# Performance work log

Hardware: AMD Instinct MI355X
Metric: run time of the kernel (lower is better)

## Reference

```python
import jax, jax.numpy as jnp
import numpy as np

K_NEIGH = 16  # ball-query neighborhood size


def pdist2(a, b):
    # (B,N,3),(B,M,3) -> (B,N,M) squared euclidean distances
    aa = jnp.sum(a * a, -1)[:, :, None]
    bb = jnp.sum(b * b, -1)[:, None, :]
    return jnp.maximum(aa + bb - 2.0 * jnp.einsum('bnd,bmd->bnm', a, b), 0.0)


def fps(xyz, npoint):
    # furthest point sampling, xyz (B,N,3) -> idx (B,npoint) int32
    B, N, _ = xyz.shape

    def body(carry, _):
        dist, far = carry
        centroid = xyz[jnp.arange(B), far]  # (B,3)
        d = jnp.sum((xyz - centroid[:, None, :]) ** 2, -1)
        dist = jnp.minimum(dist, d)
        nxt = jnp.argmax(dist, axis=1).astype(jnp.int32)
        return (dist, nxt), far

    init = (jnp.full((B, N), 1e10, xyz.dtype), jnp.zeros((B,), jnp.int32))
    _, idxs = jax.lax.scan(body, init, None, length=npoint)
    return idxs.T  # (B, npoint)


def gather(x, idx):
    # x (B,N,C), idx (B,S) -> (B,S,C)
    return jnp.take_along_axis(x, idx[:, :, None], axis=1)


def lae_conv(xyz, fea, W, b, A, radius):
    # LAE-Conv: ball-query (K nearest capped to radius, out-of-ball -> self),
    # pointwise feature transform, attention over neighbors from coord offsets.
    B, N, _ = xyz.shape
    d2 = pdist2(xyz, xyz)
    negd, idx = jax.lax.top_k(-d2, K_NEIGH)          # (B,N,K)
    in_ball = (-negd) <= radius * radius
    self_idx = jnp.broadcast_to(jnp.arange(N, dtype=idx.dtype)[None, :, None], idx.shape)
    idx = jnp.where(in_ball, idx, self_idx)
    g_xyz = jnp.take_along_axis(xyz[:, None], idx[..., None], axis=2) - xyz[:, :, None, :]  # (B,N,K,3)
    g_fea = jnp.take_along_axis(fea[:, None], idx[..., None], axis=2)                        # (B,N,K,Cin)
    h = jnp.einsum('bnkc,co->bnko', g_fea, W) + b    # (B,N,K,Cout)
    alpha = jax.nn.softmax(jnp.einsum('bnkd,d->bnk', g_xyz, A), axis=-1)
    return jax.nn.relu(jnp.einsum('bnk,bnko->bno', alpha, h))


def self_attn(fea, Wq, Wk, Wv):
    # non-local self-attention block with additive merge (PSAB)
    q, k, v = fea @ Wq, fea @ Wk, fea @ Wv
    a = jax.nn.softmax(jnp.einsum('bnc,bmc->bnm', q, k), axis=-1)
    return jnp.einsum('bnm,bmc->bnc', a, v) + fea


def fp_interp(xyz_d, xyz_s, fea_d, fea_s):
    # pointnet feature propagation: 3-NN inverse-distance interp + skip concat
    d2 = pdist2(xyz_d, xyz_s)
    negd, idx = jax.lax.top_k(-d2, 3)
    w = 1.0 / jnp.maximum(-negd, 1e-10)
    w = w / jnp.sum(w, -1, keepdims=True)
    g = jnp.take_along_axis(fea_s[:, None], idx[..., None], axis=2)  # (B,Nd,3,C)
    interp = jnp.einsum('bnk,bnkc->bnc', w, g)
    return jnp.concatenate([fea_d, interp], axis=-1)


def pan_forward(xyz, W0, b0, A0, W1, b1, A1, W2, b2, A2, W3, b3, A3, W4, b4, A4,
                W5, b5, A5, W6, b6, A6, Wq1, Wk1, Wv1, Wq2, Wk2, Wv2, Wq3, Wk3, Wv3, Wf, bf):
    fea0 = lae_conv(xyz, xyz, W0, b0, A0, 0.06)       # (B,N,64)
    idx1 = fps(xyz, 512)
    xyz1, fea1 = gather(xyz, idx1), gather(fea0, idx1)
    fea1 = lae_conv(xyz1, fea1, W1, b1, A1, 0.12)     # (B,512,128)
    idx2 = fps(xyz1, 128)
    xyz2, fea2 = gather(xyz1, idx2), gather(fea1, idx2)
    fea2 = lae_conv(xyz2, fea2, W2, b2, A2, 0.3)      # (B,128,256)
    fea2 = self_attn(fea2, Wq1, Wk1, Wv1)
    idx3 = fps(xyz2, 64)
    xyz3, fea3 = gather(xyz2, idx3), gather(fea2, idx3)
    fea3 = lae_conv(xyz3, fea3, W3, b3, A3, 0.5)      # (B,64,512)
    fea3 = self_attn(fea3, Wq2, Wk2, Wv2)
    fea2 = fp_interp(xyz2, xyz3, fea2, fea3)          # (B,128,768)
    fea2 = lae_conv(xyz2, fea2, W4, b4, A4, 0.3)      # (B,128,256)
    fea2 = self_attn(fea2, Wq3, Wk3, Wv3)
    fea1 = fp_interp(xyz1, xyz2, fea1, fea2)          # (B,512,384)
    fea1 = lae_conv(xyz1, fea1, W5, b5, A5, 0.12)     # (B,512,256)
    fea0 = fp_interp(xyz, xyz1, fea0, fea1)           # (B,N,320)
    fea0 = lae_conv(xyz, fea0, W6, b6, A6, 0.06)      # (B,N,128)
    out = fea0 @ Wf + bf                              # (B,N,num_class)
    return out.transpose(0, 2, 1)                     # (B,num_class,N)


def setup_inputs() -> dict:
    key = jax.random.key(0)
    B, N, NUM_CLASS = 4, 4096, 13
    ks = iter(jax.random.split(key, 64))

    def lin(cin, cout):
        return jax.random.normal(next(ks), (cin, cout), jnp.float32) / np.sqrt(cin).astype(np.float32)

    inp = {'xyz': jax.random.uniform(next(ks), (B, N, 3), jnp.float32)}
    lae_dims = [(3, 64), (64, 128), (128, 256), (256, 512), (768, 256), (384, 256), (320, 128)]
    for i, (ci, co) in enumerate(lae_dims):
        inp[f'W{i}'] = lin(ci, co)
        inp[f'b{i}'] = jnp.zeros((co,), jnp.float32)
        inp[f'A{i}'] = jax.random.normal(next(ks), (3,), jnp.float32)
    for j, c in zip((1, 2, 3), (256, 512, 256)):
        inp[f'Wq{j}'] = lin(c, c)
        inp[f'Wk{j}'] = lin(c, c)
        inp[f'Wv{j}'] = lin(c, c)
    inp['Wf'] = lin(128, NUM_CLASS)
    inp['bf'] = jnp.zeros((NUM_CLASS,), jnp.float32)
    return inp


def reference(xyz, W0, b0, A0, W1, b1, A1, W2, b2, A2, W3, b3, A3, W4, b4, A4,
              W5, b5, A5, W6, b6, A6, Wq1, Wk1, Wv1, Wq2, Wk2, Wv2, Wq3, Wk3, Wv3, Wf, bf):
    return pan_forward(xyz, W0, b0, A0, W1, b1, A1, W2, b2, A2, W3, b3, A3, W4, b4, A4,
                       W5, b5, A5, W6, b6, A6, Wq1, Wk1, Wv1, Wq2, Wk2, Wv2, Wq3, Wk3, Wv3, Wf, bf)
```

## Files before the change

### kernel.cpp

```cpp
#include <hip/hip_runtime.h>
#include <math.h>

#define NB 4

typedef unsigned long long u64;

#define CSWAP(a, b)                                          \
  {                                                          \
    u64 _mn = (b < a) ? b : a;                               \
    u64 _mx = (b < a) ? a : b;                               \
    a = _mn;                                                 \
    b = _mx;                                                 \
  }

__device__ __forceinline__ void knn16_search(const float* __restrict__ xb, int N, int n,
                                             int lane, u64* lists, u64* win) {
#pragma clang fp contract(off)
  float qx = xb[n * 3 + 0], qy = xb[n * 3 + 1], qz = xb[n * 3 + 2];
  float qq = qx * qx + qy * qy + qz * qz;
  const u64 SENT = ((u64)0x7F800000u << 32) | (unsigned)lane;
  u64 k0 = SENT, k1 = SENT, k2 = SENT, k3 = SENT, k4 = SENT, k5 = SENT, k6 = SENT,
      k7 = SENT, k8 = SENT, k9 = SENT, k10 = SENT, k11 = SENT, k12 = SENT, k13 = SENT,
      k14 = SENT, k15 = SENT;
  int rounds = N >> 6;
  for (int j = 0; j < rounds; ++j) {
    int m = j * 64 + lane;
    float cx = xb[m * 3 + 0], cy = xb[m * 3 + 1], cz = xb[m * 3 + 2];
    float cc = cx * cx + cy * cy + cz * cz;
    float ab = qx * cx + qy * cy + qz * cz;
    float d2 = fmaxf(qq + cc - 2.0f * ab, 0.0f);
    u64 key = ((u64)__float_as_uint(d2) << 32) | (unsigned)m;
    if (key < k15) {
      k15 = key;
      CSWAP(k14, k15); CSWAP(k13, k14); CSWAP(k12, k13); CSWAP(k11, k12);
      CSWAP(k10, k11); CSWAP(k9, k10);  CSWAP(k8, k9);   CSWAP(k7, k8);
      CSWAP(k6, k7);   CSWAP(k5, k6);   CSWAP(k4, k5);   CSWAP(k3, k4);
      CSWAP(k2, k3);   CSWAP(k1, k2);   CSWAP(k0, k1);
    }
  }
  lists[0 * 64 + lane] = k0;   lists[1 * 64 + lane] = k1;
  lists[2 * 64 + lane] = k2;   lists[3 * 64 + lane] = k3;
  lists[4 * 64 + lane] = k4;   lists[5 * 64 + lane] = k5;
  lists[6 * 64 + lane] = k6;   lists[7 * 64 + lane] = k7;
  lists[8 * 64 + lane] = k8;   lists[9 * 64 + lane] = k9;
  lists[10 * 64 + lane] = k10; lists[11 * 64 + lane] = k11;
  lists[12 * 64 + lane] = k12; lists[13 * 64 + lane] = k13;
  lists[14 * 64 + lane] = k14; lists[15 * 64 + lane] = k15;
  __syncthreads();
  int head = 0;
  u64 outk = 0;
  for (int r = 0; r < 16; ++r) {
    u64 h = lists[head * 64 + lane];
    u64 mn = h;
#pragma unroll
    for (int mask = 32; mask; mask >>= 1) {
      u64 o = __shfl_xor(mn, mask);
      if (o < mn) mn = o;
    }
    if (h == mn) head++;
    if (lane == r) outk = mn;
  }
  if (lane < 16) win[lane] = outk;
  __syncthreads();
}

__device__ __forceinline__ void lae_alphas(const float* __restrict__ xb, int n,
                                           const int* idv, const float* __restrict__ A,
                                           float* al) {
  float ax = A[0], ay = A[1], az = A[2];
  float qx = xb[n * 3 + 0], qy = xb[n * 3 + 1], qz = xb[n * 3 + 2];
  float mx = -3.0e38f;
#pragma unroll
  for (int k = 0; k < 16; ++k) {
    float gx = xb[idv[k] * 3 + 0] - qx;
    float gy = xb[idv[k] * 3 + 1] - qy;
    float gz = xb[idv[k] * 3 + 2] - qz;
    float s = gx * ax + gy * ay + gz * az;
    al[k] = s;
    mx = fmaxf(mx, s);
  }
  float sum = 0.0f;
#pragma unroll
  for (int k = 0; k < 16; ++k) { al[k] = expf(al[k] - mx); sum += al[k]; }
#pragma unroll
  for (int k = 0; k < 16; ++k) al[k] = al[k] / sum;
}

template <int NT, int PTS, int NPT>
__device__ __forceinline__ void fps_body(const float* __restrict__ xyz, int N, int npoint,
                                         int* __restrict__ idx_out,
                                         float* __restrict__ xyz_out, u64* smem, int b,
                                         int tid) {
#pragma clang fp contract(off)
  constexpr int NW = NT / 64;
  constexpr int NG = NT / 16;
  u64* rk = smem;
  int* hist = (int*)(smem + 2 * NG);
  float* sxyz = (float*)(hist + 512);
  const float* xb = xyz + (size_t)b * N * 3;
  for (int i = tid; i < 3 * N; i += NT) sxyz[i] = xb[i];
  float px[PTS], py[PTS], pz[PTS], dist[PTS];
#pragma unroll
  for (int p = 0; p < PTS; ++p) {
    int pt = tid + p * NT;
    px[p] = xb[pt * 3 + 0];
    py[p] = xb[pt * 3 + 1];
    pz[p] = xb[pt * 3 + 2];
    dist[p] = 1e10f;
  }
  __syncthreads();
  int far = 0;
  float cx = sxyz[0], cy = sxyz[1], cz = sxyz[2];
  for (int t = 0; t < npoint; ++t) {
    if (tid == 0) hist[t] = far;
    u64 K[PTS];
#pragma unroll
    for (int p = 0; p < PTS; ++p) {
      float dx = px[p] - cx, dy = py[p] - cy, dz = pz[p] - cz;
      float d = dx * dx + dy * dy + dz * dz;
      float nd = fminf(dist[p], d);
      dist[p] = nd;
      K[p] = ((u64)__float_as_uint(nd) << 32) | (unsigned)(~(tid + p * NT));
    }
#pragma unroll
    for (int s = PTS / 2; s >= 1; s >>= 1) {
#pragma unroll
      for (int i = 0; i < s; ++i)
        if (K[i + s] > K[i]) K[i] = K[i + s];
    }
    u64 key = K[0];
#pragma unroll
    for (int m = 1; m <= 8; m <<= 1) {
      u64 o = __shfl_xor(key, m);
      if (o > key) key = o;
    }
    int par = (t & 1) * NG;
    if ((tid & 15) == 0) rk[par + (tid >> 4)] = key;
    if constexpr (NW > 1) __syncthreads();
    u64 kk = rk[par + 0];
#pragma unroll
    for (int g = 1; g < NG; ++g) {
      u64 o = rk[par + g];
      if (o > kk) kk = o;
    }
    far = (int)(~(unsigned)kk);
    cx = sxyz[3 * far + 0];
    cy = sxyz[3 * far + 1];
    cz = sxyz[3 * far + 2];
  }
  __syncthreads();
  for (int s = tid; s < npoint; s += NT) {
    int idp = hist[s];
    idx_out[(size_t)b * npoint + s] = idp;
    xyz_out[((size_t)b * npoint + s) * 3 + 0] = sxyz[3 * idp + 0];
    xyz_out[((size_t)b * npoint + s) * 3 + 1] = sxyz[3 * idp + 1];
    xyz_out[((size_t)b * npoint + s) * 3 + 2] = sxyz[3 * idp + 2];
  }
}

__device__ __forceinline__ void knn_gw_body(const float* __restrict__ xyz_s, int N, float r2,
                                            int* __restrict__ idxK,
                                            const int* __restrict__ srcmap,
                                            const float* __restrict__ fea_src, int Nsrc,
                                            int Cin, const float* __restrict__ A,
                                            float* __restrict__ wf, int bn, int lane,
                                            u64* lists, u64* win) {
  int b = bn / N, n = bn - b * N;
  const float* xb = xyz_s + (size_t)b * N * 3;
  knn16_search(xb, N, n, lane, lists, win);
  int idv[16];
#pragma unroll
  for (int k = 0; k < 16; ++k) {
    u64 kk = win[k];
    float d2 = __uint_as_float((unsigned)(kk >> 32));
    idv[k] = (d2 <= r2) ? (int)(kk & 0xFFFFFFFFu) : n;
  }
  if (lane < 16) idxK[(size_t)bn * 16 + lane] = idv[lane];
  float al[16];
  lae_alphas(xb, n, idv, A, al);
  int row[16];
  const int* sm = srcmap + (size_t)b * N;
#pragma unroll
  for (int k = 0; k < 16; ++k) row[k] = sm[idv[k]];
  const float* fb = fea_src + (size_t)b * Nsrc * Cin;
  float* wo = wf + (size_t)bn * Cin;
  for (int c = lane; c < Cin; c += 64) {
    float acc = 0.0f;
#pragma unroll
    for (int k = 0; k < 16; ++k) acc += al[k] * fb[(size_t)row[k] * Cin + c];
    wo[c] = acc;
  }
}

__device__ __forceinline__ void knn_gw0_body(const float* __restrict__ xyz, int N, float r2,
                                             int* __restrict__ idxK,
                                             const float* __restrict__ W0,
                                             const float* __restrict__ b0,
                                             const float* __restrict__ A0,
                                             float* __restrict__ fea0, int bn, int lane,
                                             u64* lists, u64* win) {
  int b = bn / N, n = bn - b * N;
  const float* xb = xyz + (size_t)b * N * 3;
  knn16_search(xb, N, n, lane, lists, win);
  int idv[16];
#pragma unroll
  for (int k = 0; k < 16; ++k) {
    u64 kk = win[k];
    float d2 = __uint_as_float((unsigned)(kk >> 32));
    idv[k] = (d2 <= r2) ? (int)(kk & 0xFFFFFFFFu) : n;
  }
  if (lane < 16) idxK[(size_t)bn * 16 + lane] = idv[lane];
  float al[16];
  lae_alphas(xb, n, idv, A0, al);
  float w0 = 0.0f, w1 = 0.0f, w2 = 0.0f;
#pragma unroll
  for (int k = 0; k < 16; ++k) {
    w0 += al[k] * xb[idv[k] * 3 + 0];
    w1 += al[k] * xb[idv[k] * 3 + 1];
    w2 += al[k] * xb[idv[k] * 3 + 2];
  }
  float v = w0 * W0[0 * 64 + lane] + w1 * W0[1 * 64 + lane] + w2 * W0[2 * 64 + lane] +
            b0[lane];
  fea0[(size_t)bn * 64 + lane] = fmaxf(v, 0.0f);
}

__device__ __forceinline__ void interp3_body(const float* __restrict__ xd,
                                             const float* __restrict__ xs, int Nd, int Ns,
                                             int* __restrict__ idx3, float* __restrict__ w3,
                                             int gid) {
#pragma clang fp contract(off)
  int b = gid / Nd;
  const float* xb = xs + (size_t)b * Ns * 3;
  float qx = xd[gid * 3 + 0], qy = xd[gid * 3 + 1], qz = xd[gid * 3 + 2];
  float qq = qx * qx + qy * qy + qz * qz;
  float v0 = 3.0e38f, v1 = 3.0e38f, v2 = 3.0e38f;
  int i0 = 0, i1 = 0, i2 = 0;
  for (int m = 0; m < Ns; ++m) {
    float cx = xb[m * 3 + 0], cy = xb[m * 3 + 1], cz = xb[m * 3 + 2];
    float cc = cx * cx + cy * cy + cz * cz;
    float ab = qx * cx + qy * cy + qz * cz;
    float d2 = fmaxf(qq + cc - 2.0f * ab, 0.0f);
    if (d2 < v2) {
      if (d2 < v0) { v2 = v1; i2 = i1; v1 = v0; i1 = i0; v0 = d2; i0 = m; }
      else if (d2 < v1) { v2 = v1; i2 = i1; v1 = d2; i1 = m; }
      else { v2 = d2; i2 = m; }
    }
  }
  float w0 = 1.0f / fmaxf(v0, 1e-10f);
  float w1 = 1.0f / fmaxf(v1, 1e-10f);
  float w2 = 1.0f / fmaxf(v2, 1e-10f);
  float s = w0 + w1 + w2;
  idx3[gid * 3 + 0] = i0; idx3[gid * 3 + 1] = i1; idx3[gid * 3 + 2] = i2;
  w3[gid * 3 + 0] = w0 / s; w3[gid * 3 + 1] = w1 / s; w3[gid * 3 + 2] = w2 / s;
}

__global__ __launch_bounds__(256) void combo_A_kernel(
    const float* __restrict__ xyz, float r2, int* __restrict__ idxK0,
    const float* __restrict__ W0, const float* __restrict__ b0,
    const float* __restrict__ A0, float* __restrict__ fea0, int* __restrict__ idx1,
    float* __restrict__ xyz1) {
  __shared__ u64 smem[6432];
  if (blockIdx.x < NB) {
    fps_body<256, 16, 4096>(xyz, 4096, 512, idx1, xyz1, smem, blockIdx.x, threadIdx.x);
  } else {
    int wave = threadIdx.x >> 6, lane = threadIdx.x & 63;
    int bn = (blockIdx.x - NB) * 4 + wave;
    knn_gw0_body(xyz, 4096, r2, idxK0, W0, b0, A0, fea0, bn, lane, smem + (size_t)wave * 1024,
                 smem + 4096 + wave * 16);
  }
}

__global__ __launch_bounds__(64) void combo_B_kernel(
    const float* __restrict__ xyz, const float* __restrict__ xyz1, float r2,
    int* __restrict__ idxK1, const int* __restrict__ idx1, const float* __restrict__ fea0,
    const float* __restrict__ A1, float* __restrict__ wf, int* __restrict__ idx2,
    float* __restrict__ xyz2, int* __restrict__ idxI0, float* __restrict__ wI0) {
  __shared__ u64 smem[1040];
  int bid = blockIdx.x;
  if (bid < NB) {
    fps_body<64, 8, 512>(xyz1, 512, 128, idx2, xyz2, smem, bid, threadIdx.x);
  } else if (bid < NB + NB * 512) {
    knn_gw_body(xyz1, 512, r2, idxK1, idx1, fea0, 4096, 64, A1, wf, bid - NB, threadIdx.x,
                smem, smem + 1024);
  } else {
    int gid = (bid - NB - NB * 512) * 64 + threadIdx.x;
    interp3_body(xyz, xyz1, 4096, 512, idxI0, wI0, gid);
  }
}

__global__ __launch_bounds__(64) void combo_D_kernel(
    const float* __restrict__ xyz1, const float* __restrict__ xyz2, float r2,
    int* __restrict__ idxK2, const int* __restrict__ idx2, const float* __restrict__ fea1,
    const float* __restrict__ A2, float* __restrict__ wf, int* __restrict__ idx3,
    float* __restrict__ xyz3, int* __restrict__ idxI1, float* __restrict__ wI1) {
  __shared__ u64 smem[1040];
  int bid = blockIdx.x;
  if (bid < NB) {
    fps_body<64, 2, 128>(xyz2, 128, 64, idx3, xyz3, smem, bid, threadIdx.x);
  } else if (bid < NB + NB * 128) {
    knn_gw_body(xyz2, 128, r2, idxK2, idx2, fea1, 512, 128, A2, wf, bid - NB, threadIdx.x,
                smem, smem + 1024);
  } else {
    int gid = (bid - NB - NB * 128) * 64 + threadIdx.x;
    interp3_body(xyz1, xyz2, 512, 128, idxI1, wI1, gid);
  }
}

__global__ __launch_bounds__(64) void combo_H_kernel(
    const float* __restrict__ xyz2, const float* __restrict__ xyz3, float r2,
    int* __restrict__ idxK3, const int* __restrict__ idx3, const float* __restrict__ fea2b,
    const float* __restrict__ A3, float* __restrict__ wf, int* __restrict__ idxI2,
    float* __restrict__ wI2) {
  __shared__ u64 smem[1040];
  int bid = blockIdx.x;
  if (bid < NB * 64) {
    knn_gw_body(xyz3, 64, r2, idxK3, idx3, fea2b, 128, 256, A3, wf, bid, threadIdx.x, smem,
                smem + 1024);
  } else {
    int gid = (bid - NB * 64) * 64 + threadIdx.x;
    interp3_body(xyz2, xyz3, 128, 64, idxI2, wI2, gid);
  }
}

__global__ __launch_bounds__(64) void gwpost_kernel(const float* __restrict__ xyz,
                                                    const float* __restrict__ Y,
                                                    const int* __restrict__ knn,
                                                    const float* __restrict__ A,
                                                    const float* __restrict__ bias,
                                                    float* __restrict__ out, int N, int C) {
  int bn = blockIdx.x;
  int b = bn / N, n = bn - b * N;
  int lane = threadIdx.x;
  const float* xb = xyz + (size_t)b * N * 3;
  const int* kn = knn + (size_t)bn * 16;
  int idv[16];
#pragma unroll
  for (int k = 0; k < 16; ++k) idv[k] = kn[k];
  float al[16];
  lae_alphas(xb, n, idv, A, al);
  const float* Yb = Y + (size_t)b * N * C;
  float* wo = out + (size_t)bn * C;
  for (int c = lane; c < C; c += 64) {
    float acc = 0.0f;
#pragma unroll
    for (int k = 0; k < 16; ++k) acc += al[k] * Yb[(size_t)idv[k] * C + c];
    wo[c] = fmaxf(acc + bias[c], 0.0f);
  }
}

__global__ __launch_bounds__(64) void gwpost_final_kernel(
    const float* __restrict__ xyz, const float* __restrict__ Y, const int* __restrict__ knn,
    const float* __restrict__ A, const float* __restrict__ bias,
    const float* __restrict__ Wf, const float* __restrict__ bfv, float* __restrict__ out,
    int N) {
  int bn = blockIdx.x;
  int b = bn / N, n = bn - b * N;
  int lane = threadIdx.x;
  const float* xb = xyz + (size_t)b * N * 3;
  const int* kn = knn + (size_t)bn * 16;
  int idv[16];
#pragma unroll
  for (int k = 0; k < 16; ++k) idv[k] = kn[k];
  float al[16];
  lae_alphas(xb, n, idv, A, al);
  const float* Yb = Y + (size_t)b * N * 128;
  float a0 = 0.0f, a1 = 0.0f;
#pragma unroll
  for (int k = 0; k < 16; ++k) {
    const float* yr = Yb + (size_t)idv[k] * 128;
    a0 += al[k] * yr[lane];
    a1 += al[k] * yr[lane + 64];
  }
  float v0 = fmaxf(a0 + bias[lane], 0.0f);
  float v1 = fmaxf(a1 + bias[lane + 64], 0.0f);
  float* ob = out + ((size_t)b * 13) * N + n;
#pragma unroll
  for (int cls = 0; cls < 13; ++cls) {
    float p = v0 * Wf[lane * 13 + cls] + v1 * Wf[(lane + 64) * 13 + cls];
#pragma unroll
    for (int m = 32; m; m >>= 1) p += __shfl_xor(p, m);
    if (lane == 0) ob[(size_t)cls * N] = p + bfv[cls];
  }
}

__device__ __forceinline__ void gemm_body(const float* __restrict__ Amat,
                                          const float* __restrict__ W,
                                          const float* __restrict__ bias,
                                          float* __restrict__ out, int K, int Cout, int relu,
                                          const int* __restrict__ i3,
                                          const float* __restrict__ w3,
                                          const float* __restrict__ Zb, int Nd, int Ns,
                                          float* lds_a) {
  int co = blockIdx.x * 64 + (threadIdx.x & 63);
  int rg = threadIdx.x >> 6;
  int r0 = blockIdx.y * 32;
  float acc[8];
#pragma unroll
  for (int j = 0; j < 8; ++j) acc[j] = 0.0f;
  for (int k0 = 0; k0 < K; k0 += 32) {
    int row = threadIdx.x >> 3;
    int kq = (threadIdx.x & 7) * 4;
    int gk = k0 + kq;
    const float* ap = Amat + (size_t)(r0 + row) * K + gk;
    float a0 = 0.0f, a1 = 0.0f, a2 = 0.0f, a3 = 0.0f;
    if (gk + 3 < K) {
      float4 tv = *(const float4*)ap;
      a0 = tv.x; a1 = tv.y; a2 = tv.z; a3 = tv.w;
    } else {
      if (gk + 0 < K) a0 = ap[0];
      if (gk + 1 < K) a1 = ap[1];
      if (gk + 2 < K) a2 = ap[2];
    }
    __syncthreads();
    lds_a[(kq + 0) * 36 + row] = a0;
    lds_a[(kq + 1) * 36 + row] = a1;
    lds_a[(kq + 2) * 36 + row] = a2;
    lds_a[(kq + 3) * 36 + row] = a3;
    __syncthreads();
    int kmax = K - k0;
    if (kmax > 32) kmax = 32;
    if (kmax == 32) {
#pragma unroll
      for (int kk = 0; kk < 32; ++kk) {
        float w = W[(size_t)(k0 + kk) * Cout + co];
        const float* ar = &lds_a[kk * 36 + rg * 8];
        float4 x0 = *(const float4*)ar;
        float4 x1 = *(const float4*)(ar + 4);
        acc[0] += x0.x * w; acc[1] += x0.y * w; acc[2] += x0.z * w; acc[3] += x0.w * w;
        acc[4] += x1.x * w; acc[5] += x1.y * w; acc[6] += x1.z * w; acc[7] += x1.w * w;
      }
    } else {
      for (int kk = 0; kk < kmax; ++kk) {
        float w = W[(size_t)(k0 + kk) * Cout + co];
        const float* ar = &lds_a[kk * 36 + rg * 8];
        float4 x0 = *(const float4*)ar;
        float4 x1 = *(const float4*)(ar + 4);
        acc[0] += x0.x * w; acc[1] += x0.y * w; acc[2] += x0.z * w; acc[3] += x0.w * w;
        acc[4] += x1.x * w; acc[5] += x1.y * w; acc[6] += x1.z * w; acc[7] += x1.w * w;
      }
    }
  }
  float bb = bias ? bias[co] : 0.0f;
#pragma unroll
  for (int j = 0; j < 8; ++j) {
    int r = r0 + rg * 8 + j;
    float vv = acc[j] + bb;
    if (i3) {
      int bidx = r / Nd;
      const int* ii = i3 + (size_t)r * 3;
      const float* ww = w3 + (size_t)r * 3;
      const float* zb = Zb + (size_t)bidx * Ns * Cout;
      vv += ww[0] * zb[(size_t)ii[0] * Cout + co] + ww[1] * zb[(size_t)ii[1] * Cout + co] +
            ww[2] * zb[(size_t)ii[2] * Cout + co];
    }
    if (relu) vv = fmaxf(vv, 0.0f);
    out[(size_t)r * Cout + co] = vv;
  }
}

__global__ __launch_bounds__(256) void gemm_kernel(const float* __restrict__ Amat,
                                                   const float* __restrict__ W,
                                                   const float* __restrict__ bias,
                                                   float* __restrict__ out, int K, int Cout,
                                                   int relu, const int* __restrict__ i3,
                                                   const float* __restrict__ w3,
                                                   const float* __restrict__ Zb, int Nd,
                                                   int Ns) {
  __shared__ float lds_a[32 * 36];
  gemm_body(Amat, W, bias, out, K, Cout, relu, i3, w3, Zb, Nd, Ns, lds_a);
}

__global__ __launch_bounds__(256) void gemm_qkv_kernel(
    const float* __restrict__ Amat, const float* __restrict__ Wq,
    const float* __restrict__ Wk, const float* __restrict__ Wv, float* __restrict__ oq,
    float* __restrict__ ok, float* __restrict__ ov, int K, int Cout) {
  __shared__ float lds_a[32 * 36];
  const float* W = blockIdx.z == 0 ? Wq : (blockIdx.z == 1 ? Wk : Wv);
  float* o = blockIdx.z == 0 ? oq : (blockIdx.z == 1 ? ok : ov);
  gemm_body(Amat, W, nullptr, o, K, Cout, 0, nullptr, nullptr, nullptr, 0, 0, lds_a);
}

__global__ __launch_bounds__(128) void attn_kernel(const float* __restrict__ q,
                                                   const float* __restrict__ k,
                                                   const float* __restrict__ v,
                                                   const float* __restrict__ fea,
                                                   float* __restrict__ out, int N, int C) {
  __shared__ float sa[128];
  __shared__ float sb[128];
  int b = blockIdx.y, n = blockIdx.x, t = threadIdx.x;
  const float* qn = q + ((size_t)b * N + n) * C;
  if (t < N) {
    const float* km = k + ((size_t)b * N + t) * C;
    float acc = 0.0f;
    for (int c = 0; c < C; ++c) acc += qn[c] * km[c];
    sa[t] = acc;
  }
  __syncthreads();
  float mx = -3.0e38f;
  for (int i = 0; i < N; ++i) mx = fmaxf(mx, sa[i]);
  if (t < N) sb[t] = expf(sa[t] - mx);
  __syncthreads();
  float sum = 0.0f;
  for (int i = 0; i < N; ++i) sum += sb[i];
  size_t rowo = ((size_t)b * N + n) * C;
  for (int c = t; c < C; c += 128) {
    float acc = 0.0f;
    for (int m = 0; m < N; ++m) acc += sb[m] * v[((size_t)b * N + m) * C + c];
    out[rowo + c] = acc / sum + fea[rowo + c];
  }
}

extern "C" void kernel_launch(void* const* d_in, const int* in_sizes, int n_in,
                              void* d_out, int out_size, void* d_ws, size_t ws_size,
                              hipStream_t stream) {
  (void)in_sizes; (void)n_in; (void)out_size; (void)ws_size;
  const float* xyz = (const float*)d_in[0];
  const float* W[7]; const float* bi[7]; const float* A[7];
  for (int i = 0; i < 7; ++i) {
    W[i] = (const float*)d_in[1 + 3 * i];
    bi[i] = (const float*)d_in[2 + 3 * i];
    A[i] = (const float*)d_in[3 + 3 * i];
  }
  const float* Wq1 = (const float*)d_in[22];
  const float* Wk1 = (const float*)d_in[23];
  const float* Wv1 = (const float*)d_in[24];
  const float* Wq2 = (const float*)d_in[25];
  const float* Wk2 = (const float*)d_in[26];
  const float* Wv2 = (const float*)d_in[27];
  const float* Wq3 = (const float*)d_in[28];
  const float* Wk3 = (const float*)d_in[29];
  const float* Wv3 = (const float*)d_in[30];
  const float* Wf = (const float*)d_in[31];
  const float* bf = (const float*)d_in[32];
  float* out = (float*)d_out;

  const int B = NB, N0 = 4096, N1 = 512, N2 = 128, N3 = 64;
  char* base = (char*)d_ws;
  size_t off = 0;
  auto alloc = [&](size_t bytes) -> void* {
    void* p = base + off;
    off += (bytes + 255) & ~(size_t)255;
    return p;
  };
  int* idxK0 = (int*)alloc((size_t)B * N0 * 16 * 4);
  int* idxK1 = (int*)alloc((size_t)B * N1 * 16 * 4);
  int* idxK2 = (int*)alloc((size_t)B * N2 * 16 * 4);
  int* idxK3 = (int*)alloc((size_t)B * N3 * 16 * 4);
  int* idx1 = (int*)alloc((size_t)B * N1 * 4);
  int* idx2 = (int*)alloc((size_t)B * N2 * 4);
  int* idx3 = (int*)alloc((size_t)B * N3 * 4);
  float* xyz1 = (float*)alloc((size_t)B * N1 * 3 * 4);
  float* xyz2 = (float*)alloc((size_t)B * N2 * 3 * 4);
  float* xyz3 = (float*)alloc((size_t)B * N3 * 3 * 4);
  float* fea0 = (float*)alloc((size_t)B * N0 * 64 * 4);
  float* fea1 = (float*)alloc((size_t)B * N1 * 128 * 4);
  float* fea1b = (float*)alloc((size_t)B * N1 * 256 * 4);
  float* fea2a = (float*)alloc((size_t)B * N2 * 256 * 4);
  float* fea2b = (float*)alloc((size_t)B * N2 * 256 * 4);
  float* fea2c = (float*)alloc((size_t)B * N2 * 256 * 4);
  float* fea2d = (float*)alloc((size_t)B * N2 * 256 * 4);
  float* fea3a = (float*)alloc((size_t)B * N3 * 512 * 4);
  float* fea3b = (float*)alloc((size_t)B * N3 * 512 * 4);
  float* qb = (float*)alloc((size_t)B * 32768 * 4);
  float* kb = (float*)alloc((size_t)B * 32768 * 4);
  float* vb = (float*)alloc((size_t)B * 32768 * 4);
  int* idxI2 = (int*)alloc((size_t)B * N2 * 3 * 4);
  float* wI2 = (float*)alloc((size_t)B * N2 * 3 * 4);
  int* idxI1 = (int*)alloc((size_t)B * N1 * 3 * 4);
  float* wI1 = (float*)alloc((size_t)B * N1 * 3 * 4);
  int* idxI0 = (int*)alloc((size_t)B * N0 * 3 * 4);
  float* wI0 = (float*)alloc((size_t)B * N0 * 3 * 4);
  float* Zb4 = (float*)alloc((size_t)B * N3 * 256 * 4);
  float* Zb5 = (float*)alloc((size_t)B * N2 * 256 * 4);
  float* Zb6 = (float*)alloc((size_t)B * N1 * 128 * 4);
  float* Y4 = (float*)alloc((size_t)B * N2 * 256 * 4);
  float* Y5 = (float*)alloc((size_t)B * N1 * 256 * 4);
  float* Y6 = (float*)alloc((size_t)B * N0 * 128 * 4);
  float* wfb = (float*)alloc((size_t)B * N0 * 320 * 4);

  float r2_0 = (float)(0.06 * 0.06);
  float r2_1 = (float)(0.12 * 0.12);
  float r2_2 = (float)(0.3 * 0.3);
  float r2_3 = (float)(0.5 * 0.5);

  combo_A_kernel<<<B + B * N0 / 4, 256, 0, stream>>>(xyz, r2_0, idxK0, W[0], bi[0], A[0],
                                                     fea0, idx1, xyz1);
  combo_B_kernel<<<B + B * N1 + B * N0 / 64, 64, 0, stream>>>(
      xyz, xyz1, r2_1, idxK1, idx1, fea0, A[1], wfb, idx2, xyz2, idxI0, wI0);
  gemm_kernel<<<dim3(2, B * N1 / 32), 256, 0, stream>>>(wfb, W[1], bi[1], fea1, 64, 128, 1,
                                                        nullptr, nullptr, nullptr, 0, 0);
  combo_D_kernel<<<B + B * N2 + B * N1 / 64, 64, 0, stream>>>(
      xyz1, xyz2, r2_2, idxK2, idx2, fea1, A[2], wfb, idx3, xyz3, idxI1, wI1);
  gemm_kernel<<<dim3(4, B * N2 / 32), 256, 0, stream>>>(wfb, W[2], bi[2], fea2a, 128, 256, 1,
                                                        nullptr, nullptr, nullptr, 0, 0);
  gemm_qkv_kernel<<<dim3(4, B * N2 / 32, 3), 256, 0, stream>>>(fea2a, Wq1, Wk1, Wv1, qb, kb,
                                                               vb, 256, 256);
  attn_kernel<<<dim3(N2, B), 128, 0, stream>>>(qb, kb, vb, fea2a, fea2b, N2, 256);

  combo_H_kernel<<<B * N3 + B * N2 / 64, 64, 0, stream>>>(xyz2, xyz3, r2_3, idxK3, idx3,
                                                          fea2b, A[3], wfb, idxI2, wI2);
  gemm_kernel<<<dim3(8, B * N3 / 32), 256, 0, stream>>>(wfb, W[3], bi[3], fea3a, 256, 512, 1,
                                                        nullptr, nullptr, nullptr, 0, 0);
  gemm_qkv_kernel<<<dim3(8, B * N3 / 32, 3), 256, 0, stream>>>(fea3a, Wq2, Wk2, Wv2, qb, kb,
                                                               vb, 512, 512);
  attn_kernel<<<dim3(N3, B), 128, 0, stream>>>(qb, kb, vb, fea3a, fea3b, N3, 512);

  gemm_kernel<<<dim3(4, B * N3 / 32), 256, 0, stream>>>(fea3b, W[4] + 256 * 256, nullptr, Zb4,
                                                        512, 256, 0, nullptr, nullptr,
                                                        nullptr, 0, 0);
  gemm_kernel<<<dim3(4, B * N2 / 32), 256, 0, stream>>>(fea2b, W[4], nullptr, Y4, 256, 256, 0,
                                                        idxI2, wI2, Zb4, N2, N3);
  gwpost_kernel<<<B * N2, 64, 0, stream>>>(xyz2, Y4, idxK2, A[4], bi[4], fea2c, N2, 256);
  gemm_qkv_kernel<<<dim3(4, B * N2 / 32, 3), 256, 0, stream>>>(fea2c, Wq3, Wk3, Wv3, qb, kb,
                                                               vb, 256, 256);
  attn_kernel<<<dim3(N2, B), 128, 0, stream>>>(qb, kb, vb, fea2c, fea2d, N2, 256);

  gemm_kernel<<<dim3(4, B * N2 / 32), 256, 0, stream>>>(fea2d, W[5] + 128 * 256, nullptr, Zb5,
                                                        256, 256, 0, nullptr, nullptr,
                                                        nullptr, 0, 0);
  gemm_kernel<<<dim3(4, B * N1 / 32), 256, 0, stream>>>(fea1, W[5], nullptr, Y5, 128, 256, 0,
                                                        idxI1, wI1, Zb5, N1, N2);
  gwpost_kernel<<<B * N1, 64, 0, stream>>>(xyz1, Y5, idxK1, A[5], bi[5], fea1b, N1, 256);

  gemm_kernel<<<dim3(2, B * N1 / 32), 256, 0, stream>>>(fea1b, W[6] + 64 * 128, nullptr, Zb6,
                                                        256, 128, 0, nullptr, nullptr,
                                                        nullptr, 0, 0);
  gemm_kernel<<<dim3(2, B * N0 / 32), 256, 0, stream>>>(fea0, W[6], nullptr, Y6, 64, 128, 0,
                                                        idxI0, wI0, Zb6, N0, N1);
  gwpost_final_kernel<<<B * N0, 64, 0, stream>>>(xyz, Y6, idxK0, A[6], bi[6], Wf, bf, out,
                                                 N0);
}
```

Baseline: 1.045 ms.

## Store point coords as padded float4 with precomputed norms; wave-level FPS reduction

Adds a pre-pass that packs xyz into float4 records holding the squared norm, and switches every kNN, interpolation, alpha and post kernel to single 16-byte loads that reuse the stored norm. FPS now reduces the argmax across the full wavefront with shuffles and only goes through shared memory between waves, which cuts LDS traffic and barriers per iteration. The attention score loop is vectorised to float4. This costs an extra kernel launch and more memory per point, and it relies on C being a multiple of 4 and the buffers being 16-byte aligned.

```diff
diff --git a/kernel.cpp b/kernel.cpp
--- a/kernel.cpp
+++ b/kernel.cpp
@@ -13,11 +13,20 @@
     b = _mx;                                                 \
   }
 
-__device__ __forceinline__ void knn16_search(const float* __restrict__ xb, int N, int n,
+__global__ __launch_bounds__(256) void norms_kernel(const float* __restrict__ xyz,
+                                                    float4* __restrict__ xw, int total) {
+#pragma clang fp contract(off)
+  int i = blockIdx.x * 256 + threadIdx.x;
+  if (i >= total) return;
+  float x = xyz[3 * i + 0], y = xyz[3 * i + 1], z = xyz[3 * i + 2];
+  xw[i] = make_float4(x, y, z, x * x + y * y + z * z);
+}
+
+__device__ __forceinline__ void knn16_search(const float4* __restrict__ xwb, int N, int n,
                                              int lane, u64* lists, u64* win) {
 #pragma clang fp contract(off)
-  float qx = xb[n * 3 + 0], qy = xb[n * 3 + 1], qz = xb[n * 3 + 2];
-  float qq = qx * qx + qy * qy + qz * qz;
+  float4 q = xwb[n];
+  float qq = q.w;
   const u64 SENT = ((u64)0x7F800000u << 32) | (unsigned)lane;
   u64 k0 = SENT, k1 = SENT, k2 = SENT, k3 = SENT, k4 = SENT, k5 = SENT, k6 = SENT,
       k7 = SENT, k8 = SENT, k9 = SENT, k10 = SENT, k11 = SENT, k12 = SENT, k13 = SENT,
@@ -25,10 +34,9 @@
   int rounds = N >> 6;
   for (int j = 0; j < rounds; ++j) {
     int m = j * 64 + lane;
-    float cx = xb[m * 3 + 0], cy = xb[m * 3 + 1], cz = xb[m * 3 + 2];
-    float cc = cx * cx + cy * cy + cz * cz;
-    float ab = qx * cx + qy * cy + qz * cz;
-    float d2 = fmaxf(qq + cc - 2.0f * ab, 0.0f);
+    float4 p = xwb[m];
+    float ab = q.x * p.x + q.y * p.y + q.z * p.z;
+    float d2 = fmaxf((qq + p.w) - 2.0f * ab, 0.0f);
     u64 key = ((u64)__float_as_uint(d2) << 32) | (unsigned)m;
     if (key < k15) {
       k15 = key;
@@ -64,17 +72,16 @@
   __syncthreads();
 }
 
-__device__ __forceinline__ void lae_alphas(const float* __restrict__ xb, int n,
+__device__ __forceinline__ void lae_alphas(const float4* __restrict__ xwb, int n,
                                            const int* idv, const float* __restrict__ A,
                                            float* al) {
   float ax = A[0], ay = A[1], az = A[2];
-  float qx = xb[n * 3 + 0], qy = xb[n * 3 + 1], qz = xb[n * 3 + 2];
+  float4 q = xwb[n];
   float mx = -3.0e38f;
 #pragma unroll
   for (int k = 0; k < 16; ++k) {
-    float gx = xb[idv[k] * 3 + 0] - qx;
-    float gy = xb[idv[k] * 3 + 1] - qy;
-    float gz = xb[idv[k] * 3 + 2] - qz;
+    float4 p = xwb[idv[k]];
+    float gx = p.x - q.x, gy = p.y - q.y, gz = p.z - q.z;
     float s = gx * ax + gy * ay + gz * az;
     al[k] = s;
     mx = fmaxf(mx, s);
@@ -87,25 +94,29 @@
 }
 
 template <int NT, int PTS, int NPT>
-__device__ __forceinline__ void fps_body(const float* __restrict__ xyz, int N, int npoint,
+__device__ __forceinline__ void fps_body(const float4* __restrict__ xw, int N, int npoint,
                                          int* __restrict__ idx_out,
-                                         float* __restrict__ xyz_out, u64* smem, int b,
+                                         float4* __restrict__ xw_out, u64* smem, int b,
                                          int tid) {
 #pragma clang fp contract(off)
   constexpr int NW = NT / 64;
-  constexpr int NG = NT / 16;
   u64* rk = smem;
-  int* hist = (int*)(smem + 2 * NG);
+  int* hist = (int*)(smem + 2 * NW);
   float* sxyz = (float*)(hist + 512);
-  const float* xb = xyz + (size_t)b * N * 3;
-  for (int i = tid; i < 3 * N; i += NT) sxyz[i] = xb[i];
+  const float4* xb = xw + (size_t)b * N;
+  for (int i = tid; i < N; i += NT) {
+    float4 p = xb[i];
+    sxyz[3 * i + 0] = p.x;
+    sxyz[3 * i + 1] = p.y;
+    sxyz[3 * i + 2] = p.z;
+  }
   float px[PTS], py[PTS], pz[PTS], dist[PTS];
 #pragma unroll
   for (int p = 0; p < PTS; ++p) {
-    int pt = tid + p * NT;
-    px[p] = xb[pt * 3 + 0];
-    py[p] = xb[pt * 3 + 1];
-    pz[p] = xb[pt * 3 + 2];
+    float4 v = xb[tid + p * NT];
+    px[p] = v.x;
+    py[p] = v.y;
+    pz[p] = v.z;
     dist[p] = 1e10f;
   }
   __syncthreads();
@@ -130,20 +141,20 @@
     }
     u64 key = K[0];
 #pragma unroll
-    for (int m = 1; m <= 8; m <<= 1) {
+    for (int m = 1; m <= 32; m <<= 1) {
       u64 o = __shfl_xor(key, m);
       if (o > key) key = o;
     }
-    int par = (t & 1) * NG;
-    if ((tid & 15) == 0) rk[par + (tid >> 4)] = key;
-    if constexpr (NW > 1) __syncthreads();
-    u64 kk = rk[par + 0];
-#pragma unroll
-    for (int g = 1; g < NG; ++g) {
-      u64 o = rk[par + g];
-      if (o > kk) kk = o;
-    }
-    far = (int)(~(unsigned)kk);
+    if constexpr (NW > 1) {
+      int par = (t & 1) * NW;
+      if ((tid & 63) == 0) rk[par + (tid >> 6)] = key;
+      __syncthreads();
+      key = rk[par + 0];
+#pragma unroll
+      for (int w = 1; w < NW; ++w)
+        if (rk[par + w] > key) key = rk[par + w];
+    }
+    far = (int)(~(unsigned)key);
     cx = sxyz[3 * far + 0];
     cy = sxyz[3 * far + 1];
     cz = sxyz[3 * far + 2];
@@ -152,13 +163,11 @@
   for (int s = tid; s < npoint; s += NT) {
     int idp = hist[s];
     idx_out[(size_t)b * npoint + s] = idp;
-    xyz_out[((size_t)b * npoint + s) * 3 + 0] = sxyz[3 * idp + 0];
-    xyz_out[((size_t)b * npoint + s) * 3 + 1] = sxyz[3 * idp + 1];
-    xyz_out[((size_t)b * npoint + s) * 3 + 2] = sxyz[3 * idp + 2];
-  }
-}
-
-__device__ __forceinline__ void knn_gw_body(const float* __restrict__ xyz_s, int N, float r2,
+    xw_out[(size_t)b * npoint + s] = xb[idp];
+  }
+}
+
+__device__ __forceinline__ void knn_gw_body(const float4* __restrict__ xw_s, int N, float r2,
                                             int* __restrict__ idxK,
                                             const int* __restrict__ srcmap,
                                             const float* __restrict__ fea_src, int Nsrc,
@@ -166,7 +175,7 @@
                                             float* __restrict__ wf, int bn, int lane,
                                             u64* lists, u64* win) {
   int b = bn / N, n = bn - b * N;
-  const float* xb = xyz_s + (size_t)b * N * 3;
+  const float4* xb = xw_s + (size_t)b * N;
   knn16_search(xb, N, n, lane, lists, win);
   int idv[16];
 #pragma unroll
@@ -192,7 +201,7 @@
   }
 }
 
-__device__ __forceinline__ void knn_gw0_body(const float* __restrict__ xyz, int N, float r2,
+__device__ __forceinline__ void knn_gw0_body(const float4* __restrict__ xw, int N, float r2,
                                              int* __restrict__ idxK,
                                              const float* __restrict__ W0,
                                              const float* __restrict__ b0,
@@ -200,7 +209,7 @@
                                              float* __restrict__ fea0, int bn, int lane,
                                              u64* lists, u64* win) {
   int b = bn / N, n = bn - b * N;
-  const float* xb = xyz + (size_t)b * N * 3;
+  const float4* xb = xw + (size_t)b * N;
   knn16_search(xb, N, n, lane, lists, win);
   int idv[16];
 #pragma unroll
@@ -215,31 +224,31 @@
   float w0 = 0.0f, w1 = 0.0f, w2 = 0.0f;
 #pragma unroll
   for (int k = 0; k < 16; ++k) {
-    w0 += al[k] * xb[idv[k] * 3 + 0];
-    w1 += al[k] * xb[idv[k] * 3 + 1];
-    w2 += al[k] * xb[idv[k] * 3 + 2];
+    float4 p = xb[idv[k]];
+    w0 += al[k] * p.x;
+    w1 += al[k] * p.y;
+    w2 += al[k] * p.z;
   }
   float v = w0 * W0[0 * 64 + lane] + w1 * W0[1 * 64 + lane] + w2 * W0[2 * 64 + lane] +
             b0[lane];
   fea0[(size_t)bn * 64 + lane] = fmaxf(v, 0.0f);
 }
 
-__device__ __forceinline__ void interp3_body(const float* __restrict__ xd,
-                                             const float* __restrict__ xs, int Nd, int Ns,
+__device__ __forceinline__ void interp3_body(const float4* __restrict__ xd,
+                                             const float4* __restrict__ xs, int Nd, int Ns,
                                              int* __restrict__ idx3, float* __restrict__ w3,
                                              int gid) {
 #pragma clang fp contract(off)
   int b = gid / Nd;
-  const float* xb = xs + (size_t)b * Ns * 3;
-  float qx = xd[gid * 3 + 0], qy = xd[gid * 3 + 1], qz = xd[gid * 3 + 2];
-  float qq = qx * qx + qy * qy + qz * qz;
+  const float4* xb = xs + (size_t)b * Ns;
+  float4 q = xd[gid];
+  float qq = q.w;
   float v0 = 3.0e38f, v1 = 3.0e38f, v2 = 3.0e38f;
   int i0 = 0, i1 = 0, i2 = 0;
   for (int m = 0; m < Ns; ++m) {
-    float cx = xb[m * 3 + 0], cy = xb[m * 3 + 1], cz = xb[m * 3 + 2];
-    float cc = cx * cx + cy * cy + cz * cz;
-    float ab = qx * cx + qy * cy + qz * cz;
-    float d2 = fmaxf(qq + cc - 2.0f * ab, 0.0f);
+    float4 p = xb[m];
+    float ab = q.x * p.x + q.y * p.y + q.z * p.z;
+    float d2 = fmaxf((qq + p.w) - 2.0f * ab, 0.0f);
     if (d2 < v2) {
       if (d2 < v0) { v2 = v1; i2 = i1; v1 = v0; i1 = i0; v0 = d2; i0 = m; }
       else if (d2 < v1) { v2 = v1; i2 = i1; v1 = d2; i1 = m; }
@@ -255,74 +264,74 @@
 }
 
 __global__ __launch_bounds__(256) void combo_A_kernel(
-    const float* __restrict__ xyz, float r2, int* __restrict__ idxK0,
+    const float4* __restrict__ xw0, float r2, int* __restrict__ idxK0,
     const float* __restrict__ W0, const float* __restrict__ b0,
     const float* __restrict__ A0, float* __restrict__ fea0, int* __restrict__ idx1,
-    float* __restrict__ xyz1) {
+    float4* __restrict__ xw1) {
   __shared__ u64 smem[6432];
   if (blockIdx.x < NB) {
-    fps_body<256, 16, 4096>(xyz, 4096, 512, idx1, xyz1, smem, blockIdx.x, threadIdx.x);
+    fps_body<256, 16, 4096>(xw0, 4096, 512, idx1, xw1, smem, blockIdx.x, threadIdx.x);
   } else {
     int wave = threadIdx.x >> 6, lane = threadIdx.x & 63;
     int bn = (blockIdx.x - NB) * 4 + wave;
-    knn_gw0_body(xyz, 4096, r2, idxK0, W0, b0, A0, fea0, bn, lane, smem + (size_t)wave * 1024,
+    knn_gw0_body(xw0, 4096, r2, idxK0, W0, b0, A0, fea0, bn, lane, smem + (size_t)wave * 1024,
                  smem + 4096 + wave * 16);
   }
 }
 
 __global__ __launch_bounds__(64) void combo_B_kernel(
-    const float* __restrict__ xyz, const float* __restrict__ xyz1, float r2,
+    const float4* __restrict__ xw0, const float4* __restrict__ xw1, float r2,
     int* __restrict__ idxK1, const int* __restrict__ idx1, const float* __restrict__ fea0,
     const float* __restrict__ A1, float* __restrict__ wf, int* __restrict__ idx2,
-    float* __restrict__ xyz2, int* __restrict__ idxI0, float* __restrict__ wI0) {
-  __shared__ u64 smem[1040];
+    float4* __restrict__ xw2, int* __restrict__ idxI0, float* __restrict__ wI0) {
+  __shared__ u64 smem[1056];
   int bid = blockIdx.x;
   if (bid < NB) {
-    fps_body<64, 8, 512>(xyz1, 512, 128, idx2, xyz2, smem, bid, threadIdx.x);
+    fps_body<64, 8, 512>(xw1, 512, 128, idx2, xw2, smem, bid, threadIdx.x);
   } else if (bid < NB + NB * 512) {
-    knn_gw_body(xyz1, 512, r2, idxK1, idx1, fea0, 4096, 64, A1, wf, bid - NB, threadIdx.x,
+    knn_gw_body(xw1, 512, r2, idxK1, idx1, fea0, 4096, 64, A1, wf, bid - NB, threadIdx.x,
                 smem, smem + 1024);
   } else {
     int gid = (bid - NB - NB * 512) * 64 + threadIdx.x;
-    interp3_body(xyz, xyz1, 4096, 512, idxI0, wI0, gid);
+    interp3_body(xw0, xw1, 4096, 512, idxI0, wI0, gid);
   }
 }
 
 __global__ __launch_bounds__(64) void combo_D_kernel(
-    const float* __restrict__ xyz1, const float* __restrict__ xyz2, float r2,
+    const float4* __restrict__ xw1, const float4* __restrict__ xw2, float r2,
     int* __restrict__ idxK2, const int* __restrict__ idx2, const float* __restrict__ fea1,
     const float* __restrict__ A2, float* __restrict__ wf, int* __restrict__ idx3,
-    float* __restrict__ xyz3, int* __restrict__ idxI1, float* __restrict__ wI1) {
-  __shared__ u64 smem[1040];
+    float4* __restrict__ xw3, int* __restrict__ idxI1, float* __restrict__ wI1) {
+  __shared__ u64 smem[1056];
   int bid = blockIdx.x;
   if (bid < NB) {
-    fps_body<64, 2, 128>(xyz2, 128, 64, idx3, xyz3, smem, bid, threadIdx.x);
+    fps_body<64, 2, 128>(xw2, 128, 64, idx3, xw3, smem, bid, threadIdx.x);
   } else if (bid < NB + NB * 128) {
-    knn_gw_body(xyz2, 128, r2, idxK2, idx2, fea1, 512, 128, A2, wf, bid - NB, threadIdx.x,
+    knn_gw_body(xw2, 128, r2, idxK2, idx2, fea1, 512, 128, A2, wf, bid - NB, threadIdx.x,
                 smem, smem + 1024);
   } else {
     int gid = (bid - NB - NB * 128) * 64 + threadIdx.x;
-    interp3_body(xyz1, xyz2, 512, 128, idxI1, wI1, gid);
+    interp3_body(xw1, xw2, 512, 128, idxI1, wI1, gid);
   }
 }
 
 __global__ __launch_bounds__(64) void combo_H_kernel(
-    const float* __restrict__ xyz2, const float* __restrict__ xyz3, float r2,
+    const float4* __restrict__ xw2, const float4* __restrict__ xw3, float r2,
     int* __restrict__ idxK3, const int* __restrict__ idx3, const float* __restrict__ fea2b,
     const float* __restrict__ A3, float* __restrict__ wf, int* __restrict__ idxI2,
     float* __restrict__ wI2) {
-  __shared__ u64 smem[1040];
+  __shared__ u64 smem[1056];
   int bid = blockIdx.x;
   if (bid < NB * 64) {
-    knn_gw_body(xyz3, 64, r2, idxK3, idx3, fea2b, 128, 256, A3, wf, bid, threadIdx.x, smem,
+    knn_gw_body(xw3, 64, r2, idxK3, idx3, fea2b, 128, 256, A3, wf, bid, threadIdx.x, smem,
                 smem + 1024);
   } else {
     int gid = (bid - NB * 64) * 64 + threadIdx.x;
-    interp3_body(xyz2, xyz3, 128, 64, idxI2, wI2, gid);
-  }
-}
-
-__global__ __launch_bounds__(64) void gwpost_kernel(const float* __restrict__ xyz,
+    interp3_body(xw2, xw3, 128, 64, idxI2, wI2, gid);
+  }
+}
+
+__global__ __launch_bounds__(64) void gwpost_kernel(const float4* __restrict__ xw,
                                                     const float* __restrict__ Y,
                                                     const int* __restrict__ knn,
                                                     const float* __restrict__ A,
@@ -331,7 +340,7 @@
   int bn = blockIdx.x;
   int b = bn / N, n = bn - b * N;
   int lane = threadIdx.x;
-  const float* xb = xyz + (size_t)b * N * 3;
+  const float4* xb = xw + (size_t)b * N;
   const int* kn = knn + (size_t)bn * 16;
   int idv[16];
 #pragma unroll
@@ -349,14 +358,14 @@
 }
 
 __global__ __launch_bounds__(64) void gwpost_final_kernel(
-    const float* __restrict__ xyz, const float* __restrict__ Y, const int* __restrict__ knn,
+    const float4* __restrict__ xw, const float* __restrict__ Y, const int* __restrict__ knn,
     const float* __restrict__ A, const float* __restrict__ bias,
     const float* __restrict__ Wf, const float* __restrict__ bfv, float* __restrict__ out,
     int N) {
   int bn = blockIdx.x;
   int b = bn / N, n = bn - b * N;
   int lane = threadIdx.x;
-  const float* xb = xyz + (size_t)b * N * 3;
+  const float4* xb = xw + (size_t)b * N;
   const int* kn = knn + (size_t)bn * 16;
   int idv[16];
 #pragma unroll
@@ -490,9 +499,15 @@
   int b = blockIdx.y, n = blockIdx.x, t = threadIdx.x;
   const float* qn = q + ((size_t)b * N + n) * C;
   if (t < N) {
-    const float* km = k + ((size_t)b * N + t) * C;
+    const float4* km = (const float4*)(k + ((size_t)b * N + t) * C);
+    const float4* q4 = (const float4*)qn;
     float acc = 0.0f;
-    for (int c = 0; c < C; ++c) acc += qn[c] * km[c];
+    int C4 = C >> 2;
+    for (int c = 0; c < C4; ++c) {
+      float4 kv = km[c];
+      float4 qv = q4[c];
+      acc += qv.x * kv.x + qv.y * kv.y + qv.z * kv.z + qv.w * kv.w;
+    }
     sa[t] = acc;
   }
   __syncthreads();
@@ -542,6 +557,10 @@
     off += (bytes + 255) & ~(size_t)255;
     return p;
   };
+  float4* xw0 = (float4*)alloc((size_t)B * N0 * 16);
+  float4* xw1 = (float4*)alloc((size_t)B * N1 * 16);
+  float4* xw2 = (float4*)alloc((size_t)B * N2 * 16);
+  float4* xw3 = (float4*)alloc((size_t)B * N3 * 16);
   int* idxK0 = (int*)alloc((size_t)B * N0 * 16 * 4);
   int* idxK1 = (int*)alloc((size_t)B * N1 * 16 * 4);
   int* idxK2 = (int*)alloc((size_t)B * N2 * 16 * 4);
@@ -549,9 +568,6 @@
   int* idx1 = (int*)alloc((size_t)B * N1 * 4);
   int* idx2 = (int*)alloc((size_t)B * N2 * 4);
   int* idx3 = (int*)alloc((size_t)B * N3 * 4);
-  float* xyz1 = (float*)alloc((size_t)B * N1 * 3 * 4);
-  float* xyz2 = (float*)alloc((size_t)B * N2 * 3 * 4);
-  float* xyz3 = (float*)alloc((size_t)B * N3 * 3 * 4);
   float* fea0 = (float*)alloc((size_t)B * N0 * 64 * 4);
   float* fea1 = (float*)alloc((size_t)B * N1 * 128 * 4);
   float* fea1b = (float*)alloc((size_t)B * N1 * 256 * 4);
@@ -583,22 +599,24 @@
   float r2_2 = (float)(0.3 * 0.3);
   float r2_3 = (float)(0.5 * 0.5);
 
-  combo_A_kernel<<<B + B * N0 / 4, 256, 0, stream>>>(xyz, r2_0, idxK0, W[0], bi[0], A[0],
-                                                     fea0, idx1, xyz1);
+  norms_kernel<<<B * N0 / 256, 256, 0, stream>>>(xyz, xw0, B * N0);
+
+  combo_A_kernel<<<B + B * N0 / 4, 256, 0, stream>>>(xw0, r2_0, idxK0, W[0], bi[0], A[0],
+                                                     fea0, idx1, xw1);
   combo_B_kernel<<<B + B * N1 + B * N0 / 64, 64, 0, stream>>>(
-      xyz, xyz1, r2_1, idxK1, idx1, fea0, A[1], wfb, idx2, xyz2, idxI0, wI0);
+      xw0, xw1, r2_1, idxK1, idx1, fea0, A[1], wfb, idx2, xw2, idxI0, wI0);
   gemm_kernel<<<dim3(2, B * N1 / 32), 256, 0, stream>>>(wfb, W[1], bi[1], fea1, 64, 128, 1,
                                                         nullptr, nullptr, nullptr, 0, 0);
   combo_D_kernel<<<B + B * N2 + B * N1 / 64, 64, 0, stream>>>(
-      xyz1, xyz2, r2_2, idxK2, idx2, fea1, A[2], wfb, idx3, xyz3, idxI1, wI1);
+      xw1, xw2, r2_2, idxK2, idx2, fea1, A[2], wfb, idx3, xw3, idxI1, wI1);
   gemm_kernel<<<dim3(4, B * N2 / 32), 256, 0, stream>>>(wfb, W[2], bi[2], fea2a, 128, 256, 1,
                                                         nullptr, nullptr, nullptr, 0, 0);
   gemm_qkv_kernel<<<dim3(4, B * N2 / 32, 3), 256, 0, stream>>>(fea2a, Wq1, Wk1, Wv1, qb, kb,
                                                                vb, 256, 256);
   attn_kernel<<<dim3(N2, B), 128, 0, stream>>>(qb, kb, vb, fea2a, fea2b, N2, 256);
 
-  combo_H_kernel<<<B * N3 + B * N2 / 64, 64, 0, stream>>>(xyz2, xyz3, r2_3, idxK3, idx3,
-                                                          fea2b, A[3], wfb, idxI2, wI2);
+  combo_H_kernel<<<B * N3 + B * N2 / 64, 64, 0, stream>>>(xw2, xw3, r2_3, idxK3, idx3, fea2b,
+                                                          A[3], wfb, idxI2, wI2);
   gemm_kernel<<<dim3(8, B * N3 / 32), 256, 0, stream>>>(wfb, W[3], bi[3], fea3a, 256, 512, 1,
                                                         nullptr, nullptr, nullptr, 0, 0);
   gemm_qkv_kernel<<<dim3(8, B * N3 / 32, 3), 256, 0, stream>>>(fea3a, Wq2, Wk2, Wv2, qb, kb,
@@ -610,7 +628,7 @@
                                                         nullptr, 0, 0);
   gemm_kernel<<<dim3(4, B * N2 / 32), 256, 0, stream>>>(fea2b, W[4], nullptr, Y4, 256, 256, 0,
                                                         idxI2, wI2, Zb4, N2, N3);
-  gwpost_kernel<<<B * N2, 64, 0, stream>>>(xyz2, Y4, idxK2, A[4], bi[4], fea2c, N2, 256);
+  gwpost_kernel<<<B * N2, 64, 0, stream>>>(xw2, Y4, idxK2, A[4], bi[4], fea2c, N2, 256);
   gemm_qkv_kernel<<<dim3(4, B * N2 / 32, 3), 256, 0, stream>>>(fea2c, Wq3, Wk3, Wv3, qb, kb,
                                                                vb, 256, 256);
   attn_kernel<<<dim3(N2, B), 128, 0, stream>>>(qb, kb, vb, fea2c, fea2d, N2, 256);
@@ -620,13 +638,13 @@
                                                         nullptr, 0, 0);
   gemm_kernel<<<dim3(4, B * N1 / 32), 256, 0, stream>>>(fea1, W[5], nullptr, Y5, 128, 256, 0,
                                                         idxI1, wI1, Zb5, N1, N2);
-  gwpost_kernel<<<B * N1, 64, 0, stream>>>(xyz1, Y5, idxK1, A[5], bi[5], fea1b, N1, 256);
+  gwpost_kernel<<<B * N1, 64, 0, stream>>>(xw1, Y5, idxK1, A[5], bi[5], fea1b, N1, 256);
 
   gemm_kernel<<<dim3(2, B * N1 / 32), 256, 0, stream>>>(fea1b, W[6] + 64 * 128, nullptr, Zb6,
                                                         256, 128, 0, nullptr, nullptr,
                                                         nullptr, 0, 0);
   gemm_kernel<<<dim3(2, B * N0 / 32), 256, 0, stream>>>(fea0, W[6], nullptr, Y6, 64, 128, 0,
                                                         idxI0, wI0, Zb6, N0, N1);
-  gwpost_final_kernel<<<B * N0, 64, 0, stream>>>(xyz, Y6, idxK0, A[6], bi[6], Wf, bf, out,
+  gwpost_final_kernel<<<B * N0, 64, 0, stream>>>(xw0, Y6, idxK0, A[6], bi[6], Wf, bf, out,
                                                  N0);
 }
```

Result: faster. 916.2 us (-12.3%).
